# Optimization experiments

Measured on AMD Instinct MI355X. Metric: run time of the kernel, lower is better.

## Reference

```python
import jax, jax.numpy as jnp
import numpy as np

EPS = 1e-5
ENC = 256  # LSTM hidden size per direction


def _conv(x, w, b):
    y = jax.lax.conv_general_dilated(x, w, (1, 1), 'VALID',
                                     dimension_numbers=('NCHW', 'OIHW', 'NCHW'))
    return y + b[None, :, None, None]


def _bn(x, g, b, m, v):
    scale = g / jnp.sqrt(v + EPS)
    return x * scale[None, :, None, None] + (b - m * scale)[None, :, None, None]


def _maxpool(x, kh, kw, sh, sw):
    return jax.lax.reduce_window(x, -jnp.inf, jax.lax.max,
                                 (1, 1, kh, kw), (1, 1, sh, sw), 'VALID')


def _lstm_dir(x, W, U, b):
    # x: (N, T, D); W: (4H, D); U: (4H, H); b: (4H,)  -- torch gate order i,f,g,o
    H = U.shape[1]
    pre = jnp.einsum('ntd,gd->tng', x, W) + b  # (T, N, 4H) precomputed input proj

    def step(carry, p):
        h, c = carry
        gates = p + h @ U.T
        i, f, g, o = jnp.split(gates, 4, axis=-1)
        c = jax.nn.sigmoid(f) * c + jax.nn.sigmoid(i) * jnp.tanh(g)
        h = jax.nn.sigmoid(o) * jnp.tanh(c)
        return (h, c), h

    N = x.shape[0]
    h0 = jnp.zeros((N, H), x.dtype)
    _, hs = jax.lax.scan(step, (h0, h0), pre)
    return jnp.swapaxes(hs, 0, 1)  # (N, T, H)


def _forward(x, c1_w, c1_b, c2_w, c2_b, c3_w, c3_b,
             bn1_g, bn1_b, bn1_m, bn1_v,
             c4_w, c4_b, c5_w, c5_b,
             bn2_g, bn2_b, bn2_m, bn2_v,
             c6_w, c6_b, bn3_g, bn3_b, bn3_m, bn3_v,
             wih_f, whh_f, bih_f, bhh_f,
             wih_b, whh_b, bih_b, bhh_b):
    y = _conv(x, c1_w, c1_b)
    y = _conv(y, c2_w, c2_b)
    y = _maxpool(y, 2, 2, 2, 2)
    y = _conv(y, c3_w, c3_b)
    y = _bn(y, bn1_g, bn1_b, bn1_m, bn1_v)
    y = _conv(y, c4_w, c4_b)
    y = _maxpool(y, 2, 2, 1, 1)
    y = _conv(y, c5_w, c5_b)
    y = _bn(y, bn2_g, bn2_b, bn2_m, bn2_v)
    y = _maxpool(y, 1, 1, 2, 2)
    y = _conv(y, c6_w, c6_b)
    y = _bn(y, bn3_g, bn3_b, bn3_m, bn3_v)
    # (bs, c, w, h) -> (bs, w, h, c)
    y = jnp.transpose(y, (0, 2, 3, 1))
    bs, w, h, c = y.shape
    # per-row LSTM with shared weights + zero init state == batch rows together
    rows = y.reshape(bs * w, h, c)
    fwd = _lstm_dir(rows, wih_f, whh_f, bih_f + bhh_f)
    bwd = _lstm_dir(rows[:, ::-1], wih_b, whh_b, bih_b + bhh_b)[:, ::-1]
    out = jnp.concatenate([fwd, bwd], axis=-1)  # (bs*w, h, 2*ENC)
    return out.reshape(bs, w * h, 2 * ENC)


def setup_inputs() -> dict:
    key = jax.random.key(0)
    ks = iter(jax.random.split(key, 40))

    def rn(shape, s=0.05):
        return jax.random.normal(next(ks), shape, dtype=jnp.float32) * s

    d = {}
    d['x'] = jax.random.normal(next(ks), (16, 3, 64, 512), dtype=jnp.float32)
    d['c1_w'] = rn((64, 3, 1, 1));    d['c1_b'] = rn((64,))
    d['c2_w'] = rn((128, 64, 3, 3));  d['c2_b'] = rn((128,))
    d['c3_w'] = rn((256, 128, 3, 3)); d['c3_b'] = rn((256,))
    d['bn1_g'] = jnp.ones((256,)); d['bn1_b'] = jnp.zeros((256,))
    d['bn1_m'] = rn((256,)); d['bn1_v'] = jax.random.uniform(next(ks), (256,), minval=0.5, maxval=1.5)
    d['c4_w'] = rn((256, 256, 3, 3)); d['c4_b'] = rn((256,))
    d['c5_w'] = rn((512, 256, 3, 3)); d['c5_b'] = rn((512,))
    d['bn2_g'] = jnp.ones((512,)); d['bn2_b'] = jnp.zeros((512,))
    d['bn2_m'] = rn((512,)); d['bn2_v'] = jax.random.uniform(next(ks), (512,), minval=0.5, maxval=1.5)
    d['c6_w'] = rn((512, 512, 3, 3)); d['c6_b'] = rn((512,))
    d['bn3_g'] = jnp.ones((512,)); d['bn3_b'] = jnp.zeros((512,))
    d['bn3_m'] = rn((512,)); d['bn3_v'] = jax.random.uniform(next(ks), (512,), minval=0.5, maxval=1.5)
    d['wih_f'] = rn((4 * ENC, 512)); d['whh_f'] = rn((4 * ENC, ENC))
    d['bih_f'] = rn((4 * ENC,));     d['bhh_f'] = rn((4 * ENC,))
    d['wih_b'] = rn((4 * ENC, 512)); d['whh_b'] = rn((4 * ENC, ENC))
    d['bih_b'] = rn((4 * ENC,));     d['bhh_b'] = rn((4 * ENC,))
    return d


def reference(x, c1_w, c1_b, c2_w, c2_b, c3_w, c3_b,
              bn1_g, bn1_b, bn1_m, bn1_v,
              c4_w, c4_b, c5_w, c5_b,
              bn2_g, bn2_b, bn2_m, bn2_v,
              c6_w, c6_b, bn3_g, bn3_b, bn3_m, bn3_v,
              wih_f, whh_f, bih_f, bhh_f,
              wih_b, whh_b, bih_b, bhh_b):
    return _forward(x, c1_w, c1_b, c2_w, c2_b, c3_w, c3_b,
                    bn1_g, bn1_b, bn1_m, bn1_v,
                    c4_w, c4_b, c5_w, c5_b,
                    bn2_g, bn2_b, bn2_m, bn2_v,
                    c6_w, c6_b, bn3_g, bn3_b, bn3_m, bn3_v,
                    wih_f, whh_f, bih_f, bhh_f,
                    wih_b, whh_b, bih_b, bhh_b)
```

## Files before the change

kernel.cpp:

```cpp
#include <hip/hip_runtime.h>
#include <cmath>

#define DEV __device__ __forceinline__

typedef __attribute__((ext_vector_type(8))) short  short8;
typedef __attribute__((ext_vector_type(8))) unsigned short ushort8;
typedef __attribute__((ext_vector_type(4))) float  f32x4;

DEV float sigm(float x){ return 1.0f/(1.0f + __expf(-x)); }
DEV float tanhx(float x){
  x = fminf(fmaxf(x, -15.0f), 15.0f);
  float e = __expf(2.0f*x);
  return (e - 1.0f)/(e + 1.0f);
}
DEV unsigned short f2bf(float f){
  unsigned u = __float_as_uint(f);
  return (unsigned short)((u + 0x7fffu + ((u>>16)&1u)) >> 16);
}
DEV float bf2f(unsigned short h){ return __uint_as_float(((unsigned)h)<<16); }
DEV void split2(float v, unsigned short& hi, unsigned short& lo){
  hi = f2bf(v); lo = f2bf(v - bf2f(hi));
}

#define GLDS(SRC, DST) __builtin_amdgcn_global_load_lds( \
  (const __attribute__((address_space(1))) unsigned int*)(SRC), \
  (__attribute__((address_space(3))) unsigned int*)(DST), 16, 0, 0)

__global__ __launch_bounds__(256) void k_fold(const float* __restrict__ w1,
    const float* __restrict__ b1, const float* __restrict__ w2,
    const float* __restrict__ b2, float* __restrict__ weff, float* __restrict__ beff)
{
  int tid = threadIdx.x;
  for (int i = tid; i < 3456; i += 256){
    int oc = i / 27, rem = i % 27, c = rem / 9, k = rem % 9;
    float s = 0.f;
    for (int m = 0; m < 64; ++m)
      s += w2[(oc*64 + m)*9 + k] * w1[m*3 + c];
    weff[i] = s;
  }
  for (int i = tid; i < 128; i += 256){
    float s = b2[i];
    for (int m = 0; m < 64; ++m){
      float t = 0.f;
      for (int k = 0; k < 9; ++k) t += w2[(i*64 + m)*9 + k];
      s += t * b1[m];
    }
    beff[i] = s;
  }
}

__global__ __launch_bounds__(256) void k_prepW(const float* __restrict__ w,
    const float* __restrict__ cb, const float* __restrict__ bng,
    const float* __restrict__ bnb, const float* __restrict__ bnm,
    const float* __restrict__ bnv, int useBN, int OC, int IC,
    unsigned short* __restrict__ WH, unsigned short* __restrict__ WL,
    float* __restrict__ bout)
{
  int idx = blockIdx.x*256 + threadIdx.x;
  int tot = OC*IC*9;
  if (idx < tot){
    int k = idx % 9; int t2 = idx/9; int ic = t2 % IC; int oc = t2/IC;
    float sc = useBN ? bng[oc]*rsqrtf(bnv[oc]+1e-5f) : 1.0f;
    unsigned short h,l; split2(w[idx]*sc, h, l);
    size_t o = ((size_t)k*OC + oc)*IC + ic;
    WH[o]=h; WL[o]=l;
  }
  if (idx < OC){
    float sc = useBN ? bng[idx]*rsqrtf(bnv[idx]+1e-5f) : 1.0f;
    float sh = useBN ? (bnb[idx]-bnm[idx]*sc) : 0.f;
    bout[idx] = cb[idx]*sc + sh;
  }
}

__global__ __launch_bounds__(256) void k_prepWg(const float* __restrict__ w,
    const float* __restrict__ b1, const float* __restrict__ b2,
    unsigned short* __restrict__ WH, unsigned short* __restrict__ WL,
    float* __restrict__ bout)
{
  int idx = blockIdx.x*256 + threadIdx.x;
  if (idx < 1024*512){
    unsigned short h,l; split2(w[idx], h, l);
    WH[idx]=h; WL[idx]=l;
  }
  if (idx < 1024) bout[idx] = b1[idx] + b2[idx];
}

__global__ __launch_bounds__(256) void k_conv2pool(const float* __restrict__ x,
    const float* __restrict__ weff, const float* __restrict__ beff,
    unsigned short* __restrict__ p1H, unsigned short* __restrict__ p1L)
{
  __shared__ float wl[8*27];
  __shared__ float sm[8][4][66];
  int tx = threadIdx.x & 63, ty = threadIdx.x >> 6;
  int ocb = blockIdx.z & 15, n = blockIdx.z >> 4;
  int oc0 = ocb*8;
  if (threadIdx.x < 216) wl[threadIdx.x] = weff[oc0*27 + threadIdx.x];
  __syncthreads();
  int ow = blockIdx.x*64 + tx;
  int oh = blockIdx.y*4 + ty;
  int owc = min(ow, 509), ohc = min(oh, 61);
  const float* xp = x + ((size_t)n*3*64 + ohc)*512 + owc;
  float iv[27];
  #pragma unroll
  for (int c = 0; c < 3; ++c)
    #pragma unroll
    for (int kh = 0; kh < 3; ++kh)
      #pragma unroll
      for (int kw = 0; kw < 3; ++kw)
        iv[c*9 + kh*3 + kw] = xp[((size_t)c*64 + kh)*512 + kw];
  #pragma unroll
  for (int j = 0; j < 8; ++j){
    float s = beff[oc0 + j];
    const float* wp = &wl[j*27];
    #pragma unroll
    for (int k = 0; k < 27; ++k) s += iv[k]*wp[k];
    sm[j][ty][tx] = s;
  }
  __syncthreads();
  int pr0 = blockIdx.y*2, pc0 = blockIdx.x*32;
  for (int i = threadIdx.x; i < 512; i += 256){
    int pc = i & 31, rem = i >> 5, q = rem & 1, j = rem >> 1;
    int prow = pr0 + q, pcol = pc0 + pc;
    if (prow < 31 && pcol < 255){
      float m0 = fmaxf(sm[j][2*q  ][2*pc], sm[j][2*q  ][2*pc+1]);
      float m1 = fmaxf(sm[j][2*q+1][2*pc], sm[j][2*q+1][2*pc+1]);
      unsigned short h,l; split2(fmaxf(m0,m1), h, l);
      size_t o = (((size_t)(n*31 + prow)*255 + pcol)<<7) + oc0 + j;
      p1H[o] = h; p1L[o] = l;
    }
  }
}

__global__ __launch_bounds__(256) void k_igemm(
    const unsigned short* __restrict__ inH, const unsigned short* __restrict__ inL,
    const unsigned short* __restrict__ wH,  const unsigned short* __restrict__ wL,
    const float* __restrict__ bias,
    unsigned short* __restrict__ outH, unsigned short* __restrict__ outL,
    float* __restrict__ outF,
    int IH, int IW, int IC, int OC, int OH, int OW,
    int K9, int sub, int nICc)
{
  __shared__ unsigned short lds[2][16384];
  const int tid  = threadIdx.x;
  const int wv   = tid >> 6, lane = tid & 63;
  const int wr   = wv >> 1,  wc   = wv & 1;
  const int kg   = lane >> 4;
  const int ocTiles = OC >> 7;
  const int ow0 = blockIdx.x << 7;
  const int oh  = blockIdx.y;
  const int ocb = blockIdx.z % ocTiles;
  const int n   = blockIdx.z / ocTiles;
  const int oc0 = ocb << 7;

  const int sp = tid >> 2, ss = tid & 3;
  size_t aBase[2], bBase[2];
  #pragma unroll
  for (int q = 0; q < 2; ++q){
    int p = q*64 + sp;
    int opix = min(ow0 + p, OW-1);
    int sw = ss ^ ((p>>1)&3);
    aBase[q] = ((size_t)(n*IH + (oh<<sub))*IW + ((size_t)opix<<sub))*IC + sw*8;
    int o = q*64 + sp;
    int swb = ss ^ ((o>>1)&3);
    bBase[q] = (size_t)(oc0 + o)*IC + swb*8;
  }
  int aoff[4], boff[4];
  #pragma unroll
  for (int mi = 0; mi < 4; ++mi){
    int pr = wr*64 + mi*16 + (lane&15);
    aoff[mi] = pr*32 + ((kg ^ ((pr>>1)&3))*8);
  }
  #pragma unroll
  for (int nj = 0; nj < 4; ++nj){
    int orow = wc*64 + nj*16 + (lane&15);
    boff[nj] = orow*32 + ((kg ^ ((orow>>1)&3))*8);
  }

  auto STAGE = [&](int buf, int kk, int ic0){
    size_t aOff = ((size_t)((kk/3)*IW + (kk%3)))*IC + ic0;
    size_t bOff = ((size_t)kk*OC)*IC + ic0;
    unsigned short* d0 = &lds[buf][wv*512];
    #pragma unroll
    for (int q = 0; q < 2; ++q){
      GLDS(inH + aBase[q] + aOff, d0 + q*2048);
      GLDS(inL + aBase[q] + aOff, d0 + 4096  + q*2048);
      GLDS(wH  + bBase[q] + bOff, d0 + 8192  + q*2048);
      GLDS(wL  + bBase[q] + bOff, d0 + 12288 + q*2048);
    }
  };

  f32x4 acc[4][4] = {};
  const int NT = K9 * nICc;
  STAGE(0, 0, 0);
  int cur = 0;
  for (int t = 0; t < NT; ++t){
    __syncthreads();
    short8 aH[4], aL[4], bH[4], bL[4];
    #pragma unroll
    for (int mi = 0; mi < 4; ++mi){
      aH[mi] = *(const short8*)&lds[cur][aoff[mi]];
      aL[mi] = *(const short8*)&lds[cur][4096 + aoff[mi]];
    }
    #pragma unroll
    for (int nj = 0; nj < 4; ++nj){
      bH[nj] = *(const short8*)&lds[cur][8192  + boff[nj]];
      bL[nj] = *(const short8*)&lds[cur][12288 + boff[nj]];
    }
    if (t+1 < NT){
      int tn = t+1, kk = tn / nICc, icc = tn - kk*nICc;
      STAGE(cur^1, kk, icc*32);
    }
    #pragma unroll
    for (int mi = 0; mi < 4; ++mi)
      #pragma unroll
      for (int nj = 0; nj < 4; ++nj){
        acc[mi][nj] = __builtin_amdgcn_mfma_f32_16x16x32_bf16(aH[mi], bH[nj], acc[mi][nj],0,0,0);
        acc[mi][nj] = __builtin_amdgcn_mfma_f32_16x16x32_bf16(aL[mi], bH[nj], acc[mi][nj],0,0,0);
        acc[mi][nj] = __builtin_amdgcn_mfma_f32_16x16x32_bf16(aH[mi], bL[nj], acc[mi][nj],0,0,0);
      }
    cur ^= 1;
  }

  const int ocL = oc0 + wc*64 + (lane&15);
  const int rb  = wr*64 + ((lane>>4)<<2);
  #pragma unroll
  for (int nj = 0; nj < 4; ++nj){
    int oc = ocL + nj*16;
    float bs = bias[oc];
    #pragma unroll
    for (int mi = 0; mi < 4; ++mi)
      #pragma unroll
      for (int j = 0; j < 4; ++j){
        int pix = ow0 + rb + mi*16 + j;
        if (pix < OW){
          size_t oi = ((size_t)(n*OH + oh)*OW + pix)*OC + oc;
          float v = acc[mi][nj][j] + bs;
          if (outF) outF[oi] = v;
          else { unsigned short h,l; split2(v,h,l); outH[oi]=h; outL[oi]=l; }
        }
      }
  }
}

__global__ __launch_bounds__(256) void k_pool2(const unsigned short* __restrict__ yH,
    const unsigned short* __restrict__ yL,
    unsigned short* __restrict__ pH, unsigned short* __restrict__ pL)
{
  int idx = blockIdx.x*256 + threadIdx.x;
  if (idx >= 1664000) return;
  int g = idx & 31; int t2 = idx >> 5;
  int pw = t2 % 250; t2 /= 250; int ph = t2 % 26; int n = t2 / 26;
  size_t base = (((size_t)(n*27 + ph)*251 + pw)<<8) + g*8;
  float v[8];
  #pragma unroll
  for (int e = 0; e < 8; ++e) v[e] = -3.4e38f;
  #pragma unroll
  for (int r = 0; r < 2; ++r)
    #pragma unroll
    for (int c = 0; c < 2; ++c){
      size_t o = base + ((size_t)(r*251 + c)<<8);
      ushort8 hv = *(const ushort8*)&yH[o];
      ushort8 lv = *(const ushort8*)&yL[o];
      #pragma unroll
      for (int e = 0; e < 8; ++e)
        v[e] = fmaxf(v[e], bf2f(hv[e]) + bf2f(lv[e]));
    }
  ushort8 oh8, ol8;
  #pragma unroll
  for (int e = 0; e < 8; ++e){ unsigned short h,l; split2(v[e],h,l); oh8[e]=h; ol8[e]=l; }
  size_t ob = (((size_t)(n*26 + ph)*250 + pw)<<8) + g*8;
  *(ushort8*)&pH[ob] = oh8;
  *(ushort8*)&pL[ob] = ol8;
}

__global__ __launch_bounds__(256) void k_transU(const float* __restrict__ Uf,
    const float* __restrict__ Ub, float* __restrict__ UT)
{
  int idx = blockIdx.x*256 + threadIdx.x;
  int d = idx >> 18; int rem = idx & 262143;
  int k = rem >> 10, g = rem & 1023;
  const float* U = d ? Ub : Uf;
  UT[idx] = U[g*256 + k];
}

__global__ __launch_bounds__(256) void k_lstm(const float* __restrict__ pre,
    const float* __restrict__ UT, float* __restrict__ out)
{
  int b = blockIdx.x;
  int dir = (b >= 80) ? 1 : 0;
  int r0 = (b - dir*80)*2;
  int j = threadIdx.x;
  const float* Ut   = UT  + (size_t)dir*262144;
  const float* preD = pre + (size_t)dir*19988480ull;
  __shared__ float h[2][256];
  h[0][j] = 0.f; h[1][j] = 0.f;
  __syncthreads();
  float c0 = 0.f, c1 = 0.f;

  for (int s = 0; s < 122; ++s){
    int t = dir ? (121 - s) : s;
    const float* p0 = preD + ((size_t)r0*122 + t)*1024 + j;
    float a00 = p0[0],      a01 = p0[256],      a02 = p0[512],      a03 = p0[768];
    float a10 = p0[124928], a11 = p0[125184],   a12 = p0[125440],   a13 = p0[125696];
    const float* up = Ut + j;
    #pragma unroll 4
    for (int k = 0; k < 256; ++k){
      float h0 = h[0][k], h1 = h[1][k];
      float u0 = up[0], u1 = up[256], u2 = up[512], u3 = up[768];
      a00 += h0*u0; a01 += h0*u1; a02 += h0*u2; a03 += h0*u3;
      a10 += h1*u0; a11 += h1*u1; a12 += h1*u2; a13 += h1*u3;
      up += 1024;
    }
    float i0 = sigm(a00), f0 = sigm(a01), g0 = tanhx(a02), o0 = sigm(a03);
    c0 = f0*c0 + i0*g0;
    float nh0 = o0*tanhx(c0);
    float i1 = sigm(a10), f1 = sigm(a11), g1 = tanhx(a12), o1 = sigm(a13);
    c1 = f1*c1 + i1*g1;
    float nh1 = o1*tanhx(c1);
    __syncthreads();
    h[0][j] = nh0; h[1][j] = nh1;
    __syncthreads();
    out[((size_t)r0*122 + t)*512 + dir*256 + j]     = nh0;
    out[((size_t)(r0+1)*122 + t)*512 + dir*256 + j] = nh1;
  }
}

extern "C" void kernel_launch(void* const* d_in, const int* in_sizes, int n_in,
                              void* d_out, int out_size, void* d_ws, size_t ws_size,
                              hipStream_t stream)
{
  const float* x    = (const float*)d_in[0];
  const float* c1w  = (const float*)d_in[1];
  const float* c1b  = (const float*)d_in[2];
  const float* c2w  = (const float*)d_in[3];
  const float* c2b  = (const float*)d_in[4];
  const float* c3w  = (const float*)d_in[5];
  const float* c3b  = (const float*)d_in[6];
  const float* bn1g = (const float*)d_in[7];
  const float* bn1b = (const float*)d_in[8];
  const float* bn1m = (const float*)d_in[9];
  const float* bn1v = (const float*)d_in[10];
  const float* c4w  = (const float*)d_in[11];
  const float* c4b  = (const float*)d_in[12];
  const float* c5w  = (const float*)d_in[13];
  const float* c5b  = (const float*)d_in[14];
  const float* bn2g = (const float*)d_in[15];
  const float* bn2b = (const float*)d_in[16];
  const float* bn2m = (const float*)d_in[17];
  const float* bn2v = (const float*)d_in[18];
  const float* c6w  = (const float*)d_in[19];
  const float* c6b  = (const float*)d_in[20];
  const float* bn3g = (const float*)d_in[21];
  const float* bn3b = (const float*)d_in[22];
  const float* bn3m = (const float*)d_in[23];
  const float* bn3v = (const float*)d_in[24];
  const float* wihf = (const float*)d_in[25];
  const float* whhf = (const float*)d_in[26];
  const float* bihf = (const float*)d_in[27];
  const float* bhhf = (const float*)d_in[28];
  const float* wihb = (const float*)d_in[29];
  const float* whhb = (const float*)d_in[30];
  const float* bihb = (const float*)d_in[31];
  const float* bhhb = (const float*)d_in[32];

  float* ws = (float*)d_ws;
  typedef unsigned short u16;

  float* pre  = ws;
  u16*   y3H  = (u16*)(ws);            u16* y3L = y3H + 15026176ull;
  u16*   y4H  = (u16*)(ws + 15100000ull); u16* y4L = y4H + 13879296ull;
  u16*   p1H  = (u16*)(ws + 29000000ull); u16* p1L = p1H + 8094720ull;
  u16*   p2H  = (u16*)(ws);            u16* p2L = p2H + 13312000ull;
  u16*   p3H  = (u16*)(ws + 15100000ull); u16* p3L = p3H + 6094848ull;
  u16*   rowsL= (u16*)(ws + 40000000ull);
  float* UT   = ws + 45100000ull;
  u16*   W3H  = (u16*)(ws + 45650000ull); u16* W3L = (u16*)(ws + 45800000ull);
  u16*   W4H  = (u16*)(ws + 45950000ull); u16* W4L = (u16*)(ws + 46250000ull);
  u16*   W5H  = (u16*)(ws + 46550000ull); u16* W5L = (u16*)(ws + 47150000ull);
  u16*   W6H  = (u16*)(ws + 47750000ull); u16* W6L = (u16*)(ws + 48950000ull);
  u16*   WgfH = (u16*)(ws + 50150000ull); u16* WgfL = (u16*)(ws + 50450000ull);
  u16*   WgbH = (u16*)(ws + 50750000ull); u16* WgbL = (u16*)(ws + 51050000ull);
  float* b3   = ws + 51350000ull;
  float* b4   = ws + 51360000ull;
  float* b5   = ws + 51370000ull;
  float* b6   = ws + 51380000ull;
  float* bgf  = ws + 51390000ull;
  float* bgb  = ws + 51400000ull;
  float* weff = ws + 51420000ull;
  float* beff = ws + 51430000ull;
  u16*   rowsH = (u16*)d_out;
  float* outF  = (float*)d_out;

  k_fold<<<1, 256, 0, stream>>>(c1w, c1b, c2w, c2b, weff, beff);
  k_prepW<<<1152, 256, 0, stream>>>(c3w, c3b, bn1g,bn1b,bn1m,bn1v, 1, 256,128, W3H,W3L, b3);
  k_prepW<<<2304, 256, 0, stream>>>(c4w, c4b, nullptr,nullptr,nullptr,nullptr, 0, 256,256, W4H,W4L, b4);
  k_prepW<<<4608, 256, 0, stream>>>(c5w, c5b, bn2g,bn2b,bn2m,bn2v, 1, 512,256, W5H,W5L, b5);
  k_prepW<<<9216, 256, 0, stream>>>(c6w, c6b, bn3g,bn3b,bn3m,bn3v, 1, 512,512, W6H,W6L, b6);
  k_prepWg<<<2048, 256, 0, stream>>>(wihf, bihf, bhhf, WgfH, WgfL, bgf);
  k_prepWg<<<2048, 256, 0, stream>>>(wihb, bihb, bhhb, WgbH, WgbL, bgb);
  k_transU<<<2048, 256, 0, stream>>>(whhf, whhb, UT);

  for (int hb = 0; hb < 2; ++hb){
    int nB = hb*8;
    const float* xh = x + (size_t)nB*98304ull;
    k_conv2pool<<<dim3(8,16,128), 256, 0, stream>>>(xh, weff, beff, p1H, p1L);
    k_igemm<<<dim3(2,29,16), 256, 0, stream>>>(p1H,p1L, W3H,W3L, b3,
        y3H,y3L, nullptr, 31,255,128,256,29,253, 9,0,4);
    k_igemm<<<dim3(2,27,16), 256, 0, stream>>>(y3H,y3L, W4H,W4L, b4,
        y4H,y4L, nullptr, 29,253,256,256,27,251, 9,0,8);
    k_pool2<<<6500, 256, 0, stream>>>(y4H,y4L, p2H,p2L);
    k_igemm<<<dim3(1,12,32), 256, 0, stream>>>(p2H,p2L, W5H,W5L, b5,
        p3H,p3L, nullptr, 26,250,256,512,12,124, 9,1,8);
    k_igemm<<<dim3(1,10,32), 256, 0, stream>>>(p3H,p3L, W6H,W6L, b6,
        rowsH + (size_t)nB*624640ull, rowsL + (size_t)nB*624640ull, nullptr,
        12,124,512,512,10,122, 9,0,16);
  }

  k_igemm<<<dim3(153,1,8), 256, 0, stream>>>(rowsH,rowsL, WgfH,WgfL, bgf,
      nullptr,nullptr, pre, 1,19520,512,1024,1,19520, 1,0,16);
  k_igemm<<<dim3(153,1,8), 256, 0, stream>>>(rowsH,rowsL, WgbH,WgbL, bgb,
      nullptr,nullptr, pre + 19988480ull, 1,19520,512,1024,1,19520, 1,0,16);

  k_lstm<<<160, 256, 0, stream>>>(pre, UT, outF);
}
```

Measured before the change: 3.244 ms.

## Spread LSTM recurrence over 1024 threads, one gate column per thread

Each LSTM block now runs 1024 threads, one per gate column, instead of 256 threads that each computed four gate columns. Each thread accumulates two rows' gate preactivations using float4 shared-memory reads of the interleaved hidden state. The results are staged in shared memory, and 512 threads then apply the nonlinearities. The aim is to cut per-thread serial work in the latency-bound recurrence, at the cost of an extra shared-memory round trip per step and idle threads during the activation phase.

After: 2.929 ms. 9.7% less time.

```diff
diff --git a/kernel.cpp b/kernel.cpp
--- a/kernel.cpp
+++ b/kernel.cpp
@@ -283,45 +283,52 @@
   UT[idx] = U[g*256 + k];
 }
 
-__global__ __launch_bounds__(256) void k_lstm(const float* __restrict__ pre,
+__global__ __launch_bounds__(1024) void k_lstm(const float* __restrict__ pre,
     const float* __restrict__ UT, float* __restrict__ out)
 {
   int b = blockIdx.x;
   int dir = (b >= 80) ? 1 : 0;
   int r0 = (b - dir*80)*2;
-  int j = threadIdx.x;
+  int g = threadIdx.x;
   const float* Ut   = UT  + (size_t)dir*262144;
   const float* preD = pre + (size_t)dir*19988480ull;
-  __shared__ float h[2][256];
-  h[0][j] = 0.f; h[1][j] = 0.f;
+  __shared__ __align__(16) float2 hsh[256];
+  __shared__ float gl[2][1024];
+  if (g < 256) hsh[g] = make_float2(0.f, 0.f);
   __syncthreads();
-  float c0 = 0.f, c1 = 0.f;
-
+  float c = 0.f;
+  const int row = g >> 8, j = g & 255;
+
+  const float* p0 = preD + ((size_t)r0*122)*1024 + g;
   for (int s = 0; s < 122; ++s){
     int t = dir ? (121 - s) : s;
-    const float* p0 = preD + ((size_t)r0*122 + t)*1024 + j;
-    float a00 = p0[0],      a01 = p0[256],      a02 = p0[512],      a03 = p0[768];
-    float a10 = p0[124928], a11 = p0[125184],   a12 = p0[125440],   a13 = p0[125696];
-    const float* up = Ut + j;
+    float a0 = p0[(size_t)t*1024];
+    float a1 = p0[(size_t)t*1024 + 124928];
+    const float* up = Ut + g;
     #pragma unroll 4
-    for (int k = 0; k < 256; ++k){
-      float h0 = h[0][k], h1 = h[1][k];
-      float u0 = up[0], u1 = up[256], u2 = up[512], u3 = up[768];
-      a00 += h0*u0; a01 += h0*u1; a02 += h0*u2; a03 += h0*u3;
-      a10 += h1*u0; a11 += h1*u1; a12 += h1*u2; a13 += h1*u3;
-      up += 1024;
-    }
-    float i0 = sigm(a00), f0 = sigm(a01), g0 = tanhx(a02), o0 = sigm(a03);
-    c0 = f0*c0 + i0*g0;
-    float nh0 = o0*tanhx(c0);
-    float i1 = sigm(a10), f1 = sigm(a11), g1 = tanhx(a12), o1 = sigm(a13);
-    c1 = f1*c1 + i1*g1;
-    float nh1 = o1*tanhx(c1);
+    for (int k = 0; k < 256; k += 2){
+      float4 hv = *(const float4*)&hsh[k];
+      float u0 = up[0];
+      float u1 = up[1024];
+      a0 = fmaf(hv.x, u0, a0);
+      a1 = fmaf(hv.y, u0, a1);
+      a0 = fmaf(hv.z, u1, a0);
+      a1 = fmaf(hv.w, u1, a1);
+      up += 2048;
+    }
+    gl[0][g] = a0; gl[1][g] = a1;
     __syncthreads();
-    h[0][j] = nh0; h[1][j] = nh1;
+    if (g < 512){
+      float i_ = sigm(gl[row][j]);
+      float f_ = sigm(gl[row][256+j]);
+      float g_ = tanhx(gl[row][512+j]);
+      float o_ = sigm(gl[row][768+j]);
+      c = f_*c + i_*g_;
+      float nh = o_*tanhx(c);
+      if (row == 0) hsh[j].x = nh; else hsh[j].y = nh;
+      out[((size_t)(r0+row)*122 + t)*512 + dir*256 + j] = nh;
+    }
     __syncthreads();
-    out[((size_t)r0*122 + t)*512 + dir*256 + j]     = nh0;
-    out[((size_t)(r0+1)*122 + t)*512 + dir*256 + j] = nh1;
   }
 }
 
@@ -421,5 +428,5 @@
   k_igemm<<<dim3(153,1,8), 256, 0, stream>>>(rowsH,rowsL, WgbH,WgbL, bgb,
       nullptr,nullptr, pre + 19988480ull, 1,19520,512,1024,1,19520, 1,0,16);
 
-  k_lstm<<<160, 256, 0, stream>>>(pre, UT, outF);
-}
+  k_lstm<<<160, 1024, 0, stream>>>(pre, UT, outF);
+}
```

## Rewrite LSTM recurrence with bf16x3 MFMA over 16-row blocks

Applied to the files above, without the earlier changes.

Replaces the scalar FP32 LSTM recurrence (2 rows per 256-thread block, 160 blocks) with a 1024-thread kernel. Each block handles 16 rows of one direction and computes h@U^T with bf16 hi/lo split MFMA instructions, stages the gate results through LDS, and feeds h back as split bf16. The recurrent weights are pre-split into hi/lo bf16 instead of being transposed in fp32. This cuts the serial per-step FMA cost, but only 20 blocks run, so most of the GPU sits idle. U is reread from global or L2 every step, and the three-term bf16 split adds a small precision risk.

Result: slower. 5.138 ms (+58.4%).

```diff
diff --git a/kernel.cpp b/kernel.cpp
--- a/kernel.cpp
+++ b/kernel.cpp
@@ -83,6 +83,18 @@
     WH[idx]=h; WL[idx]=l;
   }
   if (idx < 1024) bout[idx] = b1[idx] + b2[idx];
+}
+
+__global__ __launch_bounds__(256) void k_prepU(const float* __restrict__ Uf,
+    const float* __restrict__ Ub, unsigned short* __restrict__ UHo,
+    unsigned short* __restrict__ ULo)
+{
+  int idx = blockIdx.x*256 + threadIdx.x;
+  if (idx < 524288){
+    const float* U = (idx < 262144) ? Uf : Ub;
+    unsigned short h,l; split2(U[idx & 262143], h, l);
+    UHo[idx] = h; ULo[idx] = l;
+  }
 }
 
 __global__ __launch_bounds__(256) void k_conv2pool(const float* __restrict__ x,
@@ -273,55 +285,117 @@
   *(ushort8*)&pL[ob] = ol8;
 }
 
-__global__ __launch_bounds__(256) void k_transU(const float* __restrict__ Uf,
-    const float* __restrict__ Ub, float* __restrict__ UT)
-{
-  int idx = blockIdx.x*256 + threadIdx.x;
-  int d = idx >> 18; int rem = idx & 262143;
-  int k = rem >> 10, g = rem & 1023;
-  const float* U = d ? Ub : Uf;
-  UT[idx] = U[g*256 + k];
-}
-
-__global__ __launch_bounds__(256) void k_lstm(const float* __restrict__ pre,
-    const float* __restrict__ UT, float* __restrict__ out)
-{
-  int b = blockIdx.x;
-  int dir = (b >= 80) ? 1 : 0;
-  int r0 = (b - dir*80)*2;
-  int j = threadIdx.x;
-  const float* Ut   = UT  + (size_t)dir*262144;
-  const float* preD = pre + (size_t)dir*19988480ull;
-  __shared__ float h[2][256];
-  h[0][j] = 0.f; h[1][j] = 0.f;
+__global__ __launch_bounds__(1024) void k_lstm(const float* __restrict__ pre,
+    const unsigned short* __restrict__ UHg, const unsigned short* __restrict__ ULg,
+    float* __restrict__ out)
+{
+  __shared__ float gl[16*1028];
+  __shared__ unsigned short hAh[4096];
+  __shared__ unsigned short hAl[4096];
+  const int t   = threadIdx.x;
+  const int b   = blockIdx.x;
+  const int dir = b & 1, rbk = b >> 1;
+  const int r0  = rbk * 16;
+  const int w   = t >> 6, l = t & 63;
+  const int g0   = w * 64;
+  const int colL = l & 15, kgL = l >> 4;
+  const int lam  = (t >> 1) & 63;
+  const int grow = lam & 15;
+  const int kcG  = t >> 7;
+  const int half = t & 1;
+  const int j0   = kcG*32 + (lam >> 4)*8 + half*4;
+
+  const float* preD = pre + (size_t)dir*19988480ull
+                    + ((size_t)(r0 + grow)*122)*1024 + j0;
+  float* outD = out + ((size_t)(r0 + grow)*122)*512 + dir*256 + j0;
+  const unsigned short* bptH = UHg + (size_t)dir*262144 + (size_t)(g0 + colL)*256 + kgL*8;
+  const unsigned short* bptL = ULg + (size_t)dir*262144 + (size_t)(g0 + colL)*256 + kgL*8;
+  const int hIdx = kcG*512 + lam*8 + half*4;
+
+  {
+    uint2 z{0,0};
+    *(uint2*)&hAh[t*4] = z;
+    *(uint2*)&hAl[t*4] = z;
+  }
   __syncthreads();
-  float c0 = 0.f, c1 = 0.f;
+
+  float c0 = 0.f, c1 = 0.f, c2 = 0.f, c3 = 0.f;
 
   for (int s = 0; s < 122; ++s){
-    int t = dir ? (121 - s) : s;
-    const float* p0 = preD + ((size_t)r0*122 + t)*1024 + j;
-    float a00 = p0[0],      a01 = p0[256],      a02 = p0[512],      a03 = p0[768];
-    float a10 = p0[124928], a11 = p0[125184],   a12 = p0[125440],   a13 = p0[125696];
-    const float* up = Ut + j;
-    #pragma unroll 4
-    for (int k = 0; k < 256; ++k){
-      float h0 = h[0][k], h1 = h[1][k];
-      float u0 = up[0], u1 = up[256], u2 = up[512], u3 = up[768];
-      a00 += h0*u0; a01 += h0*u1; a02 += h0*u2; a03 += h0*u3;
-      a10 += h1*u0; a11 += h1*u1; a12 += h1*u2; a13 += h1*u3;
-      up += 1024;
-    }
-    float i0 = sigm(a00), f0 = sigm(a01), g0 = tanhx(a02), o0 = sigm(a03);
-    c0 = f0*c0 + i0*g0;
-    float nh0 = o0*tanhx(c0);
-    float i1 = sigm(a10), f1 = sigm(a11), g1 = tanhx(a12), o1 = sigm(a13);
-    c1 = f1*c1 + i1*g1;
-    float nh1 = o1*tanhx(c1);
+    const int tt = dir ? (121 - s) : s;
+    const float* pp = preD + (size_t)tt*1024;
+    float4 pg0 = *(const float4*)(pp);
+    float4 pg1 = *(const float4*)(pp + 256);
+    float4 pg2 = *(const float4*)(pp + 512);
+    float4 pg3 = *(const float4*)(pp + 768);
+
+    f32x4 acc0 = {}, acc1 = {}, acc2 = {}, acc3 = {};
+    #pragma unroll
+    for (int kc = 0; kc < 8; ++kc){
+      short8 Ah = *(const short8*)&hAh[kc*512 + l*8];
+      short8 Al = *(const short8*)&hAl[kc*512 + l*8];
+      short8 B0h = *(const short8*)(bptH +         kc*32);
+      short8 B1h = *(const short8*)(bptH +  4096 + kc*32);
+      short8 B2h = *(const short8*)(bptH +  8192 + kc*32);
+      short8 B3h = *(const short8*)(bptH + 12288 + kc*32);
+      short8 B0l = *(const short8*)(bptL +         kc*32);
+      short8 B1l = *(const short8*)(bptL +  4096 + kc*32);
+      short8 B2l = *(const short8*)(bptL +  8192 + kc*32);
+      short8 B3l = *(const short8*)(bptL + 12288 + kc*32);
+      acc0 = __builtin_amdgcn_mfma_f32_16x16x32_bf16(Ah, B0h, acc0, 0,0,0);
+      acc0 = __builtin_amdgcn_mfma_f32_16x16x32_bf16(Al, B0h, acc0, 0,0,0);
+      acc0 = __builtin_amdgcn_mfma_f32_16x16x32_bf16(Ah, B0l, acc0, 0,0,0);
+      acc1 = __builtin_amdgcn_mfma_f32_16x16x32_bf16(Ah, B1h, acc1, 0,0,0);
+      acc1 = __builtin_amdgcn_mfma_f32_16x16x32_bf16(Al, B1h, acc1, 0,0,0);
+      acc1 = __builtin_amdgcn_mfma_f32_16x16x32_bf16(Ah, B1l, acc1, 0,0,0);
+      acc2 = __builtin_amdgcn_mfma_f32_16x16x32_bf16(Ah, B2h, acc2, 0,0,0);
+      acc2 = __builtin_amdgcn_mfma_f32_16x16x32_bf16(Al, B2h, acc2, 0,0,0);
+      acc2 = __builtin_amdgcn_mfma_f32_16x16x32_bf16(Ah, B2l, acc2, 0,0,0);
+      acc3 = __builtin_amdgcn_mfma_f32_16x16x32_bf16(Ah, B3h, acc3, 0,0,0);
+      acc3 = __builtin_amdgcn_mfma_f32_16x16x32_bf16(Al, B3h, acc3, 0,0,0);
+      acc3 = __builtin_amdgcn_mfma_f32_16x16x32_bf16(Ah, B3l, acc3, 0,0,0);
+    }
+    {
+      const int rbase = kgL*4;
+      #pragma unroll
+      for (int q = 0; q < 4; ++q){
+        gl[(rbase+q)*1028 + g0 +  0 + colL] = acc0[q];
+        gl[(rbase+q)*1028 + g0 + 16 + colL] = acc1[q];
+        gl[(rbase+q)*1028 + g0 + 32 + colL] = acc2[q];
+        gl[(rbase+q)*1028 + g0 + 48 + colL] = acc3[q];
+      }
+    }
     __syncthreads();
-    h[0][j] = nh0; h[1][j] = nh1;
+
+    float4 gi = *(const float4*)&gl[grow*1028 +       j0];
+    float4 gf = *(const float4*)&gl[grow*1028 + 256 + j0];
+    float4 gg = *(const float4*)&gl[grow*1028 + 512 + j0];
+    float4 go = *(const float4*)&gl[grow*1028 + 768 + j0];
+    float h0,h1,h2,h3;
+    {
+      float i_ = sigm(gi.x + pg0.x), f_ = sigm(gf.x + pg1.x);
+      float g_ = tanhx(gg.x + pg2.x), o_ = sigm(go.x + pg3.x);
+      c0 = f_*c0 + i_*g_;  h0 = o_*tanhx(c0);
+    }{
+      float i_ = sigm(gi.y + pg0.y), f_ = sigm(gf.y + pg1.y);
+      float g_ = tanhx(gg.y + pg2.y), o_ = sigm(go.y + pg3.y);
+      c1 = f_*c1 + i_*g_;  h1 = o_*tanhx(c1);
+    }{
+      float i_ = sigm(gi.z + pg0.z), f_ = sigm(gf.z + pg1.z);
+      float g_ = tanhx(gg.z + pg2.z), o_ = sigm(go.z + pg3.z);
+      c2 = f_*c2 + i_*g_;  h2 = o_*tanhx(c2);
+    }{
+      float i_ = sigm(gi.w + pg0.w), f_ = sigm(gf.w + pg1.w);
+      float g_ = tanhx(gg.w + pg2.w), o_ = sigm(go.w + pg3.w);
+      c3 = f_*c3 + i_*g_;  h3 = o_*tanhx(c3);
+    }
+    *(float4*)(outD + (size_t)tt*512) = make_float4(h0,h1,h2,h3);
+    unsigned short hh[4], hl[4];
+    split2(h0, hh[0], hl[0]); split2(h1, hh[1], hl[1]);
+    split2(h2, hh[2], hl[2]); split2(h3, hh[3], hl[3]);
+    *(uint2*)&hAh[hIdx] = *(uint2*)hh;
+    *(uint2*)&hAl[hIdx] = *(uint2*)hl;
     __syncthreads();
-    out[((size_t)r0*122 + t)*512 + dir*256 + j]     = nh0;
-    out[((size_t)(r0+1)*122 + t)*512 + dir*256 + j] = nh1;
   }
 }
 
@@ -373,7 +447,8 @@
   u16*   p2H  = (u16*)(ws);            u16* p2L = p2H + 13312000ull;
   u16*   p3H  = (u16*)(ws + 15100000ull); u16* p3L = p3H + 6094848ull;
   u16*   rowsL= (u16*)(ws + 40000000ull);
-  float* UT   = ws + 45100000ull;
+  u16*   UHd  = (u16*)(ws + 45100000ull);
+  u16*   ULd  = (u16*)(ws + 45380000ull);
   u16*   W3H  = (u16*)(ws + 45650000ull); u16* W3L = (u16*)(ws + 45800000ull);
   u16*   W4H  = (u16*)(ws + 45950000ull); u16* W4L = (u16*)(ws + 46250000ull);
   u16*   W5H  = (u16*)(ws + 46550000ull); u16* W5L = (u16*)(ws + 47150000ull);
@@ -398,7 +473,7 @@
   k_prepW<<<9216, 256, 0, stream>>>(c6w, c6b, bn3g,bn3b,bn3m,bn3v, 1, 512,512, W6H,W6L, b6);
   k_prepWg<<<2048, 256, 0, stream>>>(wihf, bihf, bhhf, WgfH, WgfL, bgf);
   k_prepWg<<<2048, 256, 0, stream>>>(wihb, bihb, bhhb, WgbH, WgbL, bgb);
-  k_transU<<<2048, 256, 0, stream>>>(whhf, whhb, UT);
+  k_prepU<<<2048, 256, 0, stream>>>(whhf, whhb, UHd, ULd);
 
   for (int hb = 0; hb < 2; ++hb){
     int nB = hb*8;
@@ -421,5 +496,5 @@
   k_igemm<<<dim3(153,1,8), 256, 0, stream>>>(rowsH,rowsL, WgbH,WgbL, bgb,
       nullptr,nullptr, pre + 19988480ull, 1,19520,512,1024,1,19520, 1,0,16);
 
-  k_lstm<<<160, 256, 0, stream>>>(pre, UT, outF);
-}
+  k_lstm<<<20, 1024, 0, stream>>>(pre, UHd, ULd, outF);
+}
```
